# Kernel optimization log

Hardware: AMD Instinct MI355X
Metric: run time of the kernel (lower is better)

## Reference

```python
import jax, jax.numpy as jnp
import numpy as np

ROWS, COLS = 4096, 11008          # out_features, in_features
NCB, CBSIZE, CLEN = 2, 256, 8     # num_codebooks, 2**nbits, in_group_size
RANK = 32
BLOCK = ROWS                      # bolck_size = reference_weight.shape[0]
N_CODES = ROWS * COLS // CLEN     # total number of codebook entries gathered


def setup_inputs() -> dict:
    key = jax.random.key(0)
    k1, k2, k3, k4, k5 = jax.random.split(key, 5)
    codebooks = jax.random.normal(k1, (NCB, CBSIZE, CLEN), dtype=jnp.float32)
    codes = jax.random.randint(k2, (NCB, N_CODES // NCB), 0, CBSIZE, dtype=jnp.int32)
    scales = jax.random.uniform(k3, (COLS, 1), dtype=jnp.float32, minval=0.5, maxval=1.5)
    L = jax.random.normal(k4, (ROWS, RANK), dtype=jnp.float32) * 0.02
    R = jax.random.normal(k5, (RANK, COLS), dtype=jnp.float32) * 0.02
    return {"codebooks": codebooks, "codes": codes, "scales": scales, "L": L, "R": R}


def reference(codebooks, codes, scales, L, R):
    # differentiable_dequantize: per-codebook gather (embedding_bag with 1-elem
    # bags == plain gather), then per-block scale, then reshape back to weight.
    gathered = jax.vmap(lambda cb, c: cb[c])(codebooks, codes)  # (NCB, N/NCB, CLEN)
    blocks = gathered.reshape(-1, BLOCK) * scales               # (COLS, ROWS) * (COLS,1)
    dequant = blocks.reshape(ROWS, COLS)
    # low-rank correction
    return dequant + L @ R
```

## Files before the change

kernel.cpp:

```cpp
#include <hip/hip_runtime.h>
#include <hip/hip_bf16.h>

constexpr int kRows  = 4096;
constexpr int kCols  = 11008;
constexpr int kRank  = 32;
constexpr int kHalfF = 22544384;

constexpr int RT    = 32;
constexpr int CT    = 256;
constexpr int PITCH = 260;

typedef __attribute__((ext_vector_type(8))) short short8;
typedef __attribute__((ext_vector_type(4))) float f32x4;

__device__ __forceinline__ unsigned short bf16_rne(float x) {
    union { float f; unsigned u; } v; v.f = x;
    return (unsigned short)((v.u + 0x7FFFu + ((v.u >> 16) & 1u)) >> 16);
}

__global__ __launch_bounds__(256) void qw_fused(
    const float* __restrict__ codebooks,
    const int*   __restrict__ codes,
    const float* __restrict__ scales,
    const float* __restrict__ Lm,
    const float* __restrict__ Rm,
    float* __restrict__ outp)
{
    __shared__ __attribute__((aligned(16))) float cb_lds[2 * 256 * 8];
    __shared__ __attribute__((aligned(16))) float corr[RT * PITCH];

    const int tid = threadIdx.x;
    const int i0 = blockIdx.y * RT;
    const int j0 = blockIdx.x * CT;

    {
        const float4* src = (const float4*)codebooks;
        float4* dst = (float4*)cb_lds;
        #pragma unroll
        for (int t = 0; t < 4; ++t) dst[tid + t * 256] = src[tid + t * 256];
    }

    {
        const int wave = tid >> 6;
        const int lane = tid & 63;
        const int n16  = lane & 15;
        const int q    = lane >> 4;
        const int kb   = q * 8;

        const float* ap = Lm + (i0 + ((wave & 1) << 4) + n16) * kRank + kb;
        float4 a0 = *(const float4*)ap;
        float4 a1 = *(const float4*)(ap + 4);
        short8 af;
        af[0] = (short)bf16_rne(a0.x); af[1] = (short)bf16_rne(a0.y);
        af[2] = (short)bf16_rne(a0.z); af[3] = (short)bf16_rne(a0.w);
        af[4] = (short)bf16_rne(a1.x); af[5] = (short)bf16_rne(a1.y);
        af[6] = (short)bf16_rne(a1.z); af[7] = (short)bf16_rne(a1.w);

        const int row_base = ((wave & 1) << 4) + q * 4;

        #pragma unroll
        for (int nt = 0; nt < 8; ++nt) {
            const int NT  = ((wave >> 1) << 3) + nt;
            const int col = j0 + NT * 16 + n16;
            const float* bp = Rm + kb * kCols + col;
            short8 bfr;
            #pragma unroll
            for (int t = 0; t < 8; ++t)
                bfr[t] = (short)bf16_rne(bp[t * kCols]);
            f32x4 acc = {0.f, 0.f, 0.f, 0.f};
            acc = __builtin_amdgcn_mfma_f32_16x16x32_bf16(af, bfr, acc, 0, 0, 0);
            const int ccol = NT * 16 + n16;
            #pragma unroll
            for (int r = 0; r < 4; ++r)
                corr[(row_base + r) * PITCH + ccol] = acc[r];
        }
    }

    __syncthreads();

    {
        const int lane4 = (tid & 63) << 2;
        const int rbase = tid >> 6;
        #pragma unroll
        for (int p = 0; p < 8; ++p) {
            const int row = rbase + (p << 2);
            const int f = (i0 + row) * kCols + j0 + lane4;
            const int code = codes[f >> 3];
            const int cb   = (f >= kHalfF) ? 1 : 0;
            const float scale = scales[f >> 12];
            const float4 w = *(const float4*)(cb_lds + (cb << 11) + (code << 3) + (lane4 & 4));
            const float4 c = *(const float4*)(corr + row * PITCH + lane4);
            float4 o;
            o.x = w.x * scale + c.x;
            o.y = w.y * scale + c.y;
            o.z = w.z * scale + c.z;
            o.w = w.w * scale + c.w;
            *(float4*)(outp + f) = o;
        }
    }
}

extern "C" void kernel_launch(void* const* d_in, const int* in_sizes, int n_in,
                              void* d_out, int out_size, void* d_ws, size_t ws_size,
                              hipStream_t stream) {
    const float* codebooks = (const float*)d_in[0];
    const int*   codes     = (const int*)d_in[1];
    const float* scales    = (const float*)d_in[2];
    const float* Lm        = (const float*)d_in[3];
    const float* Rm        = (const float*)d_in[4];
    float* outp            = (float*)d_out;

    dim3 grid(kCols / CT, kRows / RT);
    qw_fused<<<grid, dim3(256), 0, stream>>>(codebooks, codes, scales, Lm, Rm, outp);
}
```

Before: 230.7 us.

## Prefetch codes/scales early, load one codebook per block, store correction in fp16 LDS

Each block now loads only the codebook its row range uses, cutting codebook LDS and the global copy in half. Codes and scales are prefetched into registers before the MFMA correction phase so their latency overlaps it. Each thread handles 8 contiguous outputs (one code) instead of 4. The low-rank correction is staged in LDS as fp16 instead of fp32, which halves LDS traffic but loses precision in the correction term.

Result: slower. 240.2 us (+4.1%).

```diff
diff --git a/kernel.cpp b/kernel.cpp
--- a/kernel.cpp
+++ b/kernel.cpp
@@ -4,14 +4,14 @@
 constexpr int kRows  = 4096;
 constexpr int kCols  = 11008;
 constexpr int kRank  = 32;
-constexpr int kHalfF = 22544384;
 
-constexpr int RT    = 32;
-constexpr int CT    = 256;
-constexpr int PITCH = 260;
+constexpr int RT     = 32;
+constexpr int CT     = 256;
+constexpr int CP     = 264;
 
-typedef __attribute__((ext_vector_type(8))) short short8;
-typedef __attribute__((ext_vector_type(4))) float f32x4;
+typedef __attribute__((ext_vector_type(8))) short    short8;
+typedef __attribute__((ext_vector_type(4))) float    f32x4;
+typedef __attribute__((ext_vector_type(8))) _Float16 half8;
 
 __device__ __forceinline__ unsigned short bf16_rne(float x) {
     union { float f; unsigned u; } v; v.f = x;
@@ -26,18 +26,32 @@
     const float* __restrict__ Rm,
     float* __restrict__ outp)
 {
-    __shared__ __attribute__((aligned(16))) float cb_lds[2 * 256 * 8];
-    __shared__ __attribute__((aligned(16))) float corr[RT * PITCH];
+    __shared__ __attribute__((aligned(16))) float    cb_lds[256 * 8];
+    __shared__ __attribute__((aligned(16))) _Float16 corr16[RT * CP];
 
     const int tid = threadIdx.x;
     const int i0 = blockIdx.y * RT;
     const int j0 = blockIdx.x * CT;
 
+    const int cb_flag = (i0 >= 2048) ? 1 : 0;
+
+    const int g     = tid & 31;
+    const int rbase = tid >> 5;
+    int   cd[4];
+    float sc[4];
+    #pragma unroll
+    for (int p = 0; p < 4; ++p) {
+        const int row = rbase + (p << 3);
+        const int f = (i0 + row) * kCols + j0 + (g << 3);
+        cd[p] = codes[f >> 3];
+        sc[p] = scales[f >> 12];
+    }
+
     {
-        const float4* src = (const float4*)codebooks;
+        const float4* src = (const float4*)(codebooks + (cb_flag << 11));
         float4* dst = (float4*)cb_lds;
-        #pragma unroll
-        for (int t = 0; t < 4; ++t) dst[tid + t * 256] = src[tid + t * 256];
+        dst[tid]       = src[tid];
+        dst[tid + 256] = src[tid + 256];
     }
 
     {
@@ -72,31 +86,32 @@
             const int ccol = NT * 16 + n16;
             #pragma unroll
             for (int r = 0; r < 4; ++r)
-                corr[(row_base + r) * PITCH + ccol] = acc[r];
+                corr16[(row_base + r) * CP + ccol] = (_Float16)acc[r];
         }
     }
 
     __syncthreads();
 
-    {
-        const int lane4 = (tid & 63) << 2;
-        const int rbase = tid >> 6;
-        #pragma unroll
-        for (int p = 0; p < 8; ++p) {
-            const int row = rbase + (p << 2);
-            const int f = (i0 + row) * kCols + j0 + lane4;
-            const int code = codes[f >> 3];
-            const int cb   = (f >= kHalfF) ? 1 : 0;
-            const float scale = scales[f >> 12];
-            const float4 w = *(const float4*)(cb_lds + (cb << 11) + (code << 3) + (lane4 & 4));
-            const float4 c = *(const float4*)(corr + row * PITCH + lane4);
-            float4 o;
-            o.x = w.x * scale + c.x;
-            o.y = w.y * scale + c.y;
-            o.z = w.z * scale + c.z;
-            o.w = w.w * scale + c.w;
-            *(float4*)(outp + f) = o;
-        }
+    #pragma unroll
+    for (int p = 0; p < 4; ++p) {
+        const int row = rbase + (p << 3);
+        const int f = (i0 + row) * kCols + j0 + (g << 3);
+        const float scale = sc[p];
+        const float* wsrc = cb_lds + (cd[p] << 3);
+        const float4 w0 = *(const float4*)wsrc;
+        const float4 w1 = *(const float4*)(wsrc + 4);
+        const half8 ch = *(const half8*)(corr16 + row * CP + (g << 3));
+        float4 o0, o1;
+        o0.x = w0.x * scale + (float)ch[0];
+        o0.y = w0.y * scale + (float)ch[1];
+        o0.z = w0.z * scale + (float)ch[2];
+        o0.w = w0.w * scale + (float)ch[3];
+        o1.x = w1.x * scale + (float)ch[4];
+        o1.y = w1.y * scale + (float)ch[5];
+        o1.z = w1.z * scale + (float)ch[6];
+        o1.w = w1.w * scale + (float)ch[7];
+        *(float4*)(outp + f)     = o0;
+        *(float4*)(outp + f + 4) = o1;
     }
 }
 
```
